# Kernel optimization log

Hardware: AMD Instinct MI355X
Metric: run time of the kernel (lower is better)

The kernel has to match this reference:

```python
import jax, jax.numpy as jnp
import numpy as np

N = 100000   # nodes
E = 800000   # edges
F_IN = 16
H = 64       # hidden_dim
L = 4        # num_layers
CD = 8       # contrastive_dim
BN_EPS = 1e-5


def setup_inputs() -> dict:
    key = jax.random.key(0)
    ks = jax.random.split(key, 20)
    s = 0.05
    return {
        "x": jax.random.normal(ks[0], (N, F_IN), jnp.float32),
        "edge_index": jax.random.randint(ks[1], (2, E), 0, N, jnp.int64),
        "batch": jnp.zeros((N,), jnp.int64),
        "enc_w1": jax.random.normal(ks[2], (F_IN, H), jnp.float32) * s,
        "enc_b1": jnp.zeros((H,), jnp.float32),
        "enc_w2": jax.random.normal(ks[3], (H, H), jnp.float32) * s,
        "enc_b2": jnp.zeros((H,), jnp.float32),
        "conv_w": jax.random.normal(ks[4], (L, 2 * H, H), jnp.float32) * s,
        "conv_b": jnp.zeros((L, H), jnp.float32),
        "bn_gamma": jnp.ones((L, H), jnp.float32),
        "bn_beta": jnp.zeros((L, H), jnp.float32),
        "out_w1": jax.random.normal(ks[5], (H, 64), jnp.float32) * s,
        "out_b1": jnp.zeros((64,), jnp.float32),
        "out_w2": jax.random.normal(ks[6], (64, 32), jnp.float32) * s,
        "out_b2": jnp.zeros((32,), jnp.float32),
        "out_w3": jax.random.normal(ks[7], (32, CD), jnp.float32) * s,
        "out_b3": jnp.zeros((CD,), jnp.float32),
    }


def _forward(x, edge_index, enc_w1, enc_b1, enc_w2, enc_b2,
             conv_w, conv_b, bn_gamma, bn_beta,
             out_w1, out_b1, out_w2, out_b2, out_w3, out_b3):
    row, col = edge_index[0], edge_index[1]
    # lc_encode: Linear+ELU, Linear+ELU
    h = jax.nn.elu(x @ enc_w1 + enc_b1)
    feats = jax.nn.elu(h @ enc_w2 + enc_b2)  # (N, H)

    ones = jnp.ones((E, 1), feats.dtype)
    counts = jnp.clip(jax.ops.segment_sum(ones, row, num_segments=N), 1.0)  # (N,1)
    bn_scale = 1.0 / jnp.sqrt(1.0 + BN_EPS)  # eval-mode BN: running_mean=0, running_var=1

    for i in range(L):
        xc = feats[row]               # gather centers (E, H)
        xn = feats[col]               # gather neighbors (E, H)
        ef = jnp.concatenate([xc, xn - xc], axis=-1)      # (E, 2H)
        e = jax.nn.elu(ef @ conv_w[i] + conv_b[i])        # Linear + ELU
        e = (e * bn_scale) * bn_gamma[i] + bn_beta[i]     # BatchNorm (eval); Dropout is identity
        agg = jax.ops.segment_sum(e, row, num_segments=N) / counts
        feats = agg + feats  # residual in Net.forward

    # output head (Dropout identity in eval)
    o = jax.nn.elu(feats @ out_w1 + out_b1)
    o = jax.nn.elu(o @ out_w2 + out_b2)
    return o @ out_w3 + out_b3  # (N, CD)


def reference(x, edge_index, batch, enc_w1, enc_b1, enc_w2, enc_b2,
              conv_w, conv_b, bn_gamma, bn_beta,
              out_w1, out_b1, out_w2, out_b2, out_w3, out_b3):
    out = _forward(x, edge_index, enc_w1, enc_b1, enc_w2, enc_b2,
                   conv_w, conv_b, bn_gamma, bn_beta,
                   out_w1, out_b1, out_w2, out_b2, out_w3, out_b3)
    return (out, batch)
```

## Files before the change

### kernel.cpp

```cpp
#include <hip/hip_runtime.h>

#define NN 100000
#define NE 800000
#define FIN 16
#define H 64
#define NL 4
#define CDIM 8
#define NT 1563
#define NAB 782
#define ROWS_PER_OWN 12500
#define ECHUNK 2048
#define NCHUNK ((NE + ECHUNK - 1) / ECHUNK)
#define CAP 32
#define HOT 8
#define SPILL (CAP - HOT)

typedef __attribute__((ext_vector_type(8))) short bf16x8;
typedef __attribute__((ext_vector_type(4))) float f32x4;

__device__ __forceinline__ float elu(float x) { return x > 0.f ? x : __expf(x) - 1.f; }
__device__ __forceinline__ float4 elu4(float4 v) {
    return make_float4(elu(v.x), elu(v.y), elu(v.z), elu(v.w));
}

__device__ __forceinline__ unsigned short f2bf(float x) {
    union { float f; unsigned int u; } v; v.f = x;
    unsigned int r = v.u + 0x7fffu + ((v.u >> 16) & 1u);
    return (unsigned short)(r >> 16);
}
__device__ __forceinline__ float u2f(unsigned int u) {
    union { unsigned int u; float f; } v; v.u = u;
    return v.f;
}

__global__ __launch_bounds__(256) void k_scatter(const int* __restrict__ row,
                                                 const int* __restrict__ col,
                                                 int* cnt, int* __restrict__ hot,
                                                 int* __restrict__ spill,
                                                 const float* __restrict__ convw,
                                                 unsigned short* __restrict__ WT) {
    if (blockIdx.x >= NCHUNK * 8) {
        int t = (blockIdx.x - NCHUNK * 8) * 256 + threadIdx.x;
        int i = t >> 11;
        int rem = t & 2047;
        int j = rem >> 4;
        int kg = rem & 15;
        const float* W = convw + (size_t)i * 2 * H * H;
        float v[4];
#pragma unroll
        for (int q = 0; q < 4; q++) {
            int k = kg * 4 + q;
            if (j < 64) v[q] = W[k * 64 + j] - W[(64 + k) * 64 + j];
            else        v[q] = W[(64 + k) * 64 + (j - 64)];
        }
        ushort4 p;
        p.x = f2bf(v[0]); p.y = f2bf(v[1]); p.z = f2bf(v[2]); p.w = f2bf(v[3]);
        *(ushort4*)&WT[(size_t)i * 8192 + j * 64 + kg * 4] = p;
        return;
    }
    int owner = blockIdx.x & 7;
    int chunk = blockIdx.x >> 3;
    int lo = owner * ROWS_PER_OWN, hi = lo + ROWS_PER_OWN;
    int base = chunk * ECHUNK;
    int end = base + ECHUNK; if (end > NE) end = NE;
    for (int e = base + threadIdx.x; e < end; e += 256) {
        int r = row[e];
        if (r >= lo && r < hi) {
            int p = atomicAdd(&cnt[r], 1);
            if (p < HOT) hot[(size_t)r * HOT + p] = col[e];
            else if (p < CAP) spill[(size_t)r * SPILL + (p - HOT)] = col[e];
        }
    }
}

__global__ __launch_bounds__(256) void k_enc(const float* __restrict__ x,
                                             const float* __restrict__ w1,
                                             const float* __restrict__ b1,
                                             const float* __restrict__ w2,
                                             const float* __restrict__ b2,
                                             float* __restrict__ feats,
                                             int* __restrict__ cnt) {
    __shared__ __align__(16) float xs[64 * 16];
    __shared__ __align__(16) float w1s[16 * 64];
    __shared__ __align__(16) float ws[64 * 64];
    __shared__ __align__(16) float fs[64 * 68];
    int tid = threadIdx.x;
    int base = blockIdx.x * 64;
    {
        int gid = blockIdx.x * 256 + tid;
        if (gid < NN) cnt[gid] = 0;
    }
    {
        size_t ei = (size_t)base * FIN + tid * 4;
        size_t emax = (size_t)NN * FIN - 4;
        if (ei > emax) ei = emax;
        *(float4*)&xs[tid * 4] = *(const float4*)&x[ei];
    }
    ((float4*)w1s)[tid] = ((const float4*)w1)[tid];
#pragma unroll
    for (int r = 0; r < 4; r++) ((float4*)ws)[tid + 256 * r] = ((const float4*)w2)[tid + 256 * r];
    __syncthreads();

    int wave = tid >> 6, j = tid & 63;
    float bb1 = b1[j];
    for (int i = 0; i < 16; i++) {
        int nl = i * 4 + wave;
        float acc = bb1;
#pragma unroll
        for (int k = 0; k < FIN; k++) acc += xs[nl * FIN + k] * w1s[k * 64 + j];
        fs[nl * 68 + j] = elu(acc);
    }
    __syncthreads();

    int cg = tid & 15, ng = tid >> 4;
    int c0 = cg * 4;
    float4 bb = ((const float4*)b2)[cg];
    float4 acc[4];
    acc[0] = bb; acc[1] = bb; acc[2] = bb; acc[3] = bb;
#pragma unroll 2
    for (int kq = 0; kq < 16; kq++) {
        int k0 = kq * 4;
        float4 w0 = *(const float4*)&ws[(k0 + 0) * 64 + c0];
        float4 w1v = *(const float4*)&ws[(k0 + 1) * 64 + c0];
        float4 w2v = *(const float4*)&ws[(k0 + 2) * 64 + c0];
        float4 w3v = *(const float4*)&ws[(k0 + 3) * 64 + c0];
#pragma unroll
        for (int m = 0; m < 4; m++) {
            float4 f = *(const float4*)&fs[(ng * 4 + m) * 68 + k0];
            acc[m].x += f.x * w0.x + f.y * w1v.x + f.z * w2v.x + f.w * w3v.x;
            acc[m].y += f.x * w0.y + f.y * w1v.y + f.z * w2v.y + f.w * w3v.y;
            acc[m].z += f.x * w0.z + f.y * w1v.z + f.z * w2v.z + f.w * w3v.z;
            acc[m].w += f.x * w0.w + f.y * w1v.w + f.z * w2v.w + f.w * w3v.w;
        }
    }
#pragma unroll
    for (int m = 0; m < 4; m++) {
        int n = base + ng * 4 + m;
        if (n < NN) *(float4*)&feats[(size_t)n * 64 + c0] = elu4(acc[m]);
    }
}

__global__ __launch_bounds__(256) void k_ab(const float* __restrict__ feats,
                                            const unsigned short* __restrict__ WT,
                                            const float* __restrict__ convb,
                                            unsigned short* __restrict__ Am,
                                            unsigned short* __restrict__ Bm) {
    int tid = threadIdx.x;
    int wave = tid >> 6, l = tid & 63;
    int lr = l & 15;
    int lk = l >> 4;
    int nb = blockIdx.x * 128 + wave * 32;

    bf16x8 wf[8][2];
#pragma unroll
    for (int ct = 0; ct < 8; ct++)
#pragma unroll
        for (int kt = 0; kt < 2; kt++)
            wf[ct][kt] = *(const bf16x8*)&WT[(ct * 16 + lr) * 64 + kt * 32 + lk * 8];

    f32x4 acc[2][8];
#pragma unroll
    for (int ct = 0; ct < 4; ct++) {
        float4 bq = *(const float4*)&convb[ct * 16 + lk * 4];
        f32x4 bv; bv[0] = bq.x; bv[1] = bq.y; bv[2] = bq.z; bv[3] = bq.w;
        f32x4 z = (f32x4)(0.0f);
        acc[0][ct] = bv; acc[1][ct] = bv;
        acc[0][ct + 4] = z; acc[1][ct + 4] = z;
    }

#pragma unroll
    for (int nt = 0; nt < 2; nt++) {
        int n = nb + nt * 16 + lr; if (n >= NN) n = NN - 1;
        bf16x8 ff[2];
#pragma unroll
        for (int kt = 0; kt < 2; kt++) {
            float4 f0 = *(const float4*)&feats[(size_t)n * 64 + kt * 32 + lk * 8];
            float4 f1 = *(const float4*)&feats[(size_t)n * 64 + kt * 32 + lk * 8 + 4];
            bf16x8 t;
            t[0] = (short)f2bf(f0.x); t[1] = (short)f2bf(f0.y);
            t[2] = (short)f2bf(f0.z); t[3] = (short)f2bf(f0.w);
            t[4] = (short)f2bf(f1.x); t[5] = (short)f2bf(f1.y);
            t[6] = (short)f2bf(f1.z); t[7] = (short)f2bf(f1.w);
            ff[kt] = t;
        }
#pragma unroll
        for (int ct = 0; ct < 8; ct++) {
            acc[nt][ct] = __builtin_amdgcn_mfma_f32_16x16x32_bf16(wf[ct][0], ff[0], acc[nt][ct], 0, 0, 0);
            acc[nt][ct] = __builtin_amdgcn_mfma_f32_16x16x32_bf16(wf[ct][1], ff[1], acc[nt][ct], 0, 0, 0);
        }
    }

#pragma unroll
    for (int nt = 0; nt < 2; nt++) {
        int n = nb + nt * 16 + lr;
        if (n < NN) {
#pragma unroll
            for (int ct = 0; ct < 8; ct++) {
                ushort4 p;
                p.x = f2bf(acc[nt][ct][0]); p.y = f2bf(acc[nt][ct][1]);
                p.z = f2bf(acc[nt][ct][2]); p.w = f2bf(acc[nt][ct][3]);
                unsigned short* dst = (ct < 4) ? Am : Bm;
                int wc = (ct & 3) * 16 + lk * 4;
                *(ushort4*)&dst[(size_t)n * 64 + wc] = p;
            }
        }
    }
}

__global__ __launch_bounds__(256) void k_gather(const unsigned short* __restrict__ Am,
                                                const unsigned short* __restrict__ Bm,
                                                const int* __restrict__ cnt,
                                                const int* __restrict__ hot,
                                                const int* __restrict__ spill,
                                                const float* __restrict__ gamma,
                                                const float* __restrict__ beta,
                                                float* __restrict__ feats) {
    int tid = threadIdx.x;
    int wave = tid >> 6, lane = tid & 63;
    int half = lane >> 5, l = lane & 31;
    int n = blockIdx.x * 8 + wave * 2 + half;
    int g = l >> 3;
    int cq = l & 7, c0 = cq * 8;
    int deg = cnt[n];
    if (deg > CAP) deg = CAP;
    int mycol = (l < HOT) ? hot[(size_t)n * HOT + l]
                          : spill[(size_t)n * SPILL + (l - HOT)];
    uint4 rawA = *(const uint4*)&Am[(size_t)n * H + c0];
    float4 a0 = make_float4(u2f(rawA.x << 16), u2f(rawA.x & 0xffff0000u),
                            u2f(rawA.y << 16), u2f(rawA.y & 0xffff0000u));
    float4 a1 = make_float4(u2f(rawA.z << 16), u2f(rawA.z & 0xffff0000u),
                            u2f(rawA.w << 16), u2f(rawA.w & 0xffff0000u));
    float4 f0, f1;
    if (g == 0) {
        f0 = *(const float4*)&feats[(size_t)n * H + c0];
        f1 = *(const float4*)&feats[(size_t)n * H + c0 + 4];
    }
    float4 acc0 = make_float4(0.f, 0.f, 0.f, 0.f);
    float4 acc1 = make_float4(0.f, 0.f, 0.f, 0.f);
    for (int p0 = 0; p0 < deg; p0 += 4) {
        int p = p0 + g;
        bool valid = p < deg;
        int pc = valid ? p : (deg - 1);
        int c = __shfl(mycol, (half << 5) + pc);
        uint4 raw = *(const uint4*)&Bm[(size_t)c * H + c0];
        float4 b0 = make_float4(u2f(raw.x << 16), u2f(raw.x & 0xffff0000u),
                                u2f(raw.y << 16), u2f(raw.y & 0xffff0000u));
        float4 b1 = make_float4(u2f(raw.z << 16), u2f(raw.z & 0xffff0000u),
                                u2f(raw.w << 16), u2f(raw.w & 0xffff0000u));
        float4 v0 = elu4(make_float4(a0.x + b0.x, a0.y + b0.y, a0.z + b0.z, a0.w + b0.w));
        float4 v1 = elu4(make_float4(a1.x + b1.x, a1.y + b1.y, a1.z + b1.z, a1.w + b1.w));
        if (valid) {
            acc0.x += v0.x; acc0.y += v0.y; acc0.z += v0.z; acc0.w += v0.w;
            acc1.x += v1.x; acc1.y += v1.y; acc1.z += v1.z; acc1.w += v1.w;
        }
    }
#pragma unroll
    for (int d = 8; d < 32; d <<= 1) {
        acc0.x += __shfl_xor(acc0.x, d); acc0.y += __shfl_xor(acc0.y, d);
        acc0.z += __shfl_xor(acc0.z, d); acc0.w += __shfl_xor(acc0.w, d);
        acc1.x += __shfl_xor(acc1.x, d); acc1.y += __shfl_xor(acc1.y, d);
        acc1.z += __shfl_xor(acc1.z, d); acc1.w += __shfl_xor(acc1.w, d);
    }
    if (g == 0 && deg > 0) {
        const float bs = 0.99999500003749968750f;
        float inv = bs / (float)deg;
        float4 gm0 = *(const float4*)&gamma[c0];
        float4 gm1 = *(const float4*)&gamma[c0 + 4];
        float4 bt0 = *(const float4*)&beta[c0];
        float4 bt1 = *(const float4*)&beta[c0 + 4];
        f0.x += acc0.x * gm0.x * inv + bt0.x;
        f0.y += acc0.y * gm0.y * inv + bt0.y;
        f0.z += acc0.z * gm0.z * inv + bt0.z;
        f0.w += acc0.w * gm0.w * inv + bt0.w;
        f1.x += acc1.x * gm1.x * inv + bt1.x;
        f1.y += acc1.y * gm1.y * inv + bt1.y;
        f1.z += acc1.z * gm1.z * inv + bt1.z;
        f1.w += acc1.w * gm1.w * inv + bt1.w;
        *(float4*)&feats[(size_t)n * H + c0] = f0;
        *(float4*)&feats[(size_t)n * H + c0 + 4] = f1;
    }
}

__global__ __launch_bounds__(256) void k_head(const float* __restrict__ feats,
                                              const float* __restrict__ w1,
                                              const float* __restrict__ b1,
                                              const float* __restrict__ w2,
                                              const float* __restrict__ b2,
                                              const float* __restrict__ w3,
                                              const float* __restrict__ b3,
                                              const int* __restrict__ batch,
                                              float* __restrict__ out,
                                              float* __restrict__ out2) {
    __shared__ __align__(16) float fs[64 * 68];
    __shared__ __align__(16) float w1s[64 * 64];
    __shared__ __align__(16) float o1s[64 * 68];
    __shared__ __align__(16) float w2s[64 * 32];
    __shared__ __align__(16) float w3s[32 * 8];
    int tid = threadIdx.x;
    int base = blockIdx.x * 64;
#pragma unroll
    for (int r = 0; r < 4; r++) {
        int idx = tid + 256 * r;
        ((float4*)w1s)[idx] = ((const float4*)w1)[idx];
        int rw = idx >> 4, cc = idx & 15;
        int n = base + rw; if (n >= NN) n = NN - 1;
        *(float4*)&fs[rw * 68 + cc * 4] = *(const float4*)&feats[(size_t)n * 64 + cc * 4];
    }
    ((float4*)w2s)[tid] = ((const float4*)w2)[tid];
    ((float4*)w2s)[tid + 256] = ((const float4*)w2)[tid + 256];
    if (tid < 64) ((float4*)w3s)[tid] = ((const float4*)w3)[tid];
    if (tid < 64) {
        int n = base + tid;
        if (n < NN) out2[n] = (float)batch[n];
    }
    __syncthreads();

    int cg = tid & 15, ng = tid >> 4;
    int c0 = cg * 4;
    {
        float4 bb = ((const float4*)b1)[cg];
        float4 acc[4];
        acc[0] = bb; acc[1] = bb; acc[2] = bb; acc[3] = bb;
#pragma unroll 2
        for (int kq = 0; kq < 16; kq++) {
            int k0 = kq * 4;
            float4 w0 = *(const float4*)&w1s[(k0 + 0) * 64 + c0];
            float4 w1v = *(const float4*)&w1s[(k0 + 1) * 64 + c0];
            float4 w2v = *(const float4*)&w1s[(k0 + 2) * 64 + c0];
            float4 w3v = *(const float4*)&w1s[(k0 + 3) * 64 + c0];
#pragma unroll
            for (int m = 0; m < 4; m++) {
                float4 f = *(const float4*)&fs[(ng * 4 + m) * 68 + k0];
                acc[m].x += f.x * w0.x + f.y * w1v.x + f.z * w2v.x + f.w * w3v.x;
                acc[m].y += f.x * w0.y + f.y * w1v.y + f.z * w2v.y + f.w * w3v.y;
                acc[m].z += f.x * w0.z + f.y * w1v.z + f.z * w2v.z + f.w * w3v.z;
                acc[m].w += f.x * w0.w + f.y * w1v.w + f.z * w2v.w + f.w * w3v.w;
            }
        }
        __syncthreads();
#pragma unroll
        for (int m = 0; m < 4; m++)
            *(float4*)&o1s[(ng * 4 + m) * 68 + c0] = elu4(acc[m]);
    }
    __syncthreads();

    float* o2s = fs;
    {
        int cg2 = tid & 7, ng2 = tid >> 3;
        int c20 = cg2 * 4;
        float4 bb = ((const float4*)b2)[cg2];
        float4 acc[2];
        acc[0] = bb; acc[1] = bb;
#pragma unroll 2
        for (int kq = 0; kq < 16; kq++) {
            int k0 = kq * 4;
            float4 w0 = *(const float4*)&w2s[(k0 + 0) * 32 + c20];
            float4 w1v = *(const float4*)&w2s[(k0 + 1) * 32 + c20];
            float4 w2v = *(const float4*)&w2s[(k0 + 2) * 32 + c20];
            float4 w3v = *(const float4*)&w2s[(k0 + 3) * 32 + c20];
#pragma unroll
            for (int m = 0; m < 2; m++) {
                float4 f = *(const float4*)&o1s[(ng2 * 2 + m) * 68 + k0];
                acc[m].x += f.x * w0.x + f.y * w1v.x + f.z * w2v.x + f.w * w3v.x;
                acc[m].y += f.x * w0.y + f.y * w1v.y + f.z * w2v.y + f.w * w3v.y;
                acc[m].z += f.x * w0.z + f.y * w1v.z + f.z * w2v.z + f.w * w3v.z;
                acc[m].w += f.x * w0.w + f.y * w1v.w + f.z * w2v.w + f.w * w3v.w;
            }
        }
#pragma unroll
        for (int m = 0; m < 2; m++)
            *(float4*)&o2s[(ng2 * 2 + m) * 40 + c20] = elu4(acc[m]);
    }
    __syncthreads();

    if (tid < 128) {
        int n3 = tid >> 1, c30 = (tid & 1) * 4;
        float4 acc = ((const float4*)b3)[tid & 1];
#pragma unroll 2
        for (int kq = 0; kq < 8; kq++) {
            int k0 = kq * 4;
            float4 w0 = *(const float4*)&w3s[(k0 + 0) * 8 + c30];
            float4 w1v = *(const float4*)&w3s[(k0 + 1) * 8 + c30];
            float4 w2v = *(const float4*)&w3s[(k0 + 2) * 8 + c30];
            float4 w3v = *(const float4*)&w3s[(k0 + 3) * 8 + c30];
            float4 f = *(const float4*)&o2s[n3 * 40 + k0];
            acc.x += f.x * w0.x + f.y * w1v.x + f.z * w2v.x + f.w * w3v.x;
            acc.y += f.x * w0.y + f.y * w1v.y + f.z * w2v.y + f.w * w3v.y;
            acc.z += f.x * w0.z + f.y * w1v.z + f.z * w2v.z + f.w * w3v.z;
            acc.w += f.x * w0.w + f.y * w1v.w + f.z * w2v.w + f.w * w3v.w;
        }
        int n = base + n3;
        if (n < NN) *(float4*)&out[(size_t)n * 8 + c30] = acc;
    }
}

extern "C" void kernel_launch(void* const* d_in, const int* in_sizes, int n_in,
                              void* d_out, int out_size, void* d_ws, size_t ws_size,
                              hipStream_t stream) {
    const float* x = (const float*)d_in[0];
    const int* edge_index = (const int*)d_in[1];
    const int* batch = (const int*)d_in[2];
    const float* enc_w1 = (const float*)d_in[3];
    const float* enc_b1 = (const float*)d_in[4];
    const float* enc_w2 = (const float*)d_in[5];
    const float* enc_b2 = (const float*)d_in[6];
    const float* conv_w = (const float*)d_in[7];
    const float* conv_b = (const float*)d_in[8];
    const float* bn_gamma = (const float*)d_in[9];
    const float* bn_beta = (const float*)d_in[10];
    const float* out_w1 = (const float*)d_in[11];
    const float* out_b1 = (const float*)d_in[12];
    const float* out_w2 = (const float*)d_in[13];
    const float* out_b2 = (const float*)d_in[14];
    const float* out_w3 = (const float*)d_in[15];
    const float* out_b3 = (const float*)d_in[16];

    const int* row = edge_index;
    const int* col = edge_index + NE;

    float* feats = (float*)d_ws;
    unsigned short* Abuf = (unsigned short*)(feats + (size_t)NN * H);
    unsigned short* Bbuf = Abuf + (size_t)NN * H;
    int* cnt = (int*)(Bbuf + (size_t)NN * H);
    int* hot = cnt + NN;
    int* spill = hot + (size_t)NN * HOT;
    unsigned short* WT = (unsigned short*)(spill + (size_t)NN * SPILL);

    float* out = (float*)d_out;

    k_enc<<<NT, 256, 0, stream>>>(x, enc_w1, enc_b1, enc_w2, enc_b2, feats, cnt);
    k_scatter<<<NCHUNK * 8 + 32, 256, 0, stream>>>(row, col, cnt, hot, spill, conv_w, WT);

    for (int i = 0; i < NL; i++) {
        k_ab<<<NAB, 256, 0, stream>>>(feats, WT + (size_t)i * 8192,
                                      conv_b + (size_t)i * H, Abuf, Bbuf);
        k_gather<<<NN / 8, 256, 0, stream>>>(Abuf, Bbuf, cnt, hot, spill,
                                             bn_gamma + (size_t)i * H,
                                             bn_beta + (size_t)i * H, feats);
    }

    k_head<<<NT, 256, 0, stream>>>(feats, out_w1, out_b1, out_w2, out_b2,
                                   out_w3, out_b3, batch, out,
                                   out + (size_t)NN * CDIM);
}
```

Measured before the change: 383.6 us.

## Fuse neighbor aggregation with next layer's A/B projection, double-buffering B

A new kernel, k_gab, does layer i's neighbor gather, mean, BN and residual update for a 128-node tile. After a barrier it computes layer i+1's A/B bf16 projections for the same tile. B is ping-ponged between two buffers because other blocks still read the old B as neighbor values, while A and feats are only touched by their owning tile. The conv weight transpose also moves from k_scatter into extra blocks of k_enc. This saves a few launches and one re-read of feats per layer. The cost is far fewer, longer-running blocks in the gather phase, each wave walking 32 nodes serially, which may hide less gather latency.

```diff
diff --git a/kernel.cpp b/kernel.cpp
--- a/kernel.cpp
+++ b/kernel.cpp
@@ -11,6 +11,7 @@
 #define ROWS_PER_OWN 12500
 #define ECHUNK 2048
 #define NCHUNK ((NE + ECHUNK - 1) / ECHUNK)
+#define NSC (NCHUNK * 8)
 #define CAP 32
 #define HOT 8
 #define SPILL (CAP - HOT)
@@ -36,28 +37,7 @@
 __global__ __launch_bounds__(256) void k_scatter(const int* __restrict__ row,
                                                  const int* __restrict__ col,
                                                  int* cnt, int* __restrict__ hot,
-                                                 int* __restrict__ spill,
-                                                 const float* __restrict__ convw,
-                                                 unsigned short* __restrict__ WT) {
-    if (blockIdx.x >= NCHUNK * 8) {
-        int t = (blockIdx.x - NCHUNK * 8) * 256 + threadIdx.x;
-        int i = t >> 11;
-        int rem = t & 2047;
-        int j = rem >> 4;
-        int kg = rem & 15;
-        const float* W = convw + (size_t)i * 2 * H * H;
-        float v[4];
-#pragma unroll
-        for (int q = 0; q < 4; q++) {
-            int k = kg * 4 + q;
-            if (j < 64) v[q] = W[k * 64 + j] - W[(64 + k) * 64 + j];
-            else        v[q] = W[(64 + k) * 64 + (j - 64)];
-        }
-        ushort4 p;
-        p.x = f2bf(v[0]); p.y = f2bf(v[1]); p.z = f2bf(v[2]); p.w = f2bf(v[3]);
-        *(ushort4*)&WT[(size_t)i * 8192 + j * 64 + kg * 4] = p;
-        return;
-    }
+                                                 int* __restrict__ spill) {
     int owner = blockIdx.x & 7;
     int chunk = blockIdx.x >> 3;
     int lo = owner * ROWS_PER_OWN, hi = lo + ROWS_PER_OWN;
@@ -79,12 +59,33 @@
                                              const float* __restrict__ w2,
                                              const float* __restrict__ b2,
                                              float* __restrict__ feats,
-                                             int* __restrict__ cnt) {
+                                             int* __restrict__ cnt,
+                                             const float* __restrict__ convw,
+                                             unsigned short* __restrict__ WT) {
+    int tid = threadIdx.x;
+    if (blockIdx.x >= NT) {
+        int t = (blockIdx.x - NT) * 256 + tid;
+        int i = t >> 11;
+        int rem = t & 2047;
+        int j = rem >> 4;
+        int kg = rem & 15;
+        const float* W = convw + (size_t)i * 2 * H * H;
+        float v[4];
+#pragma unroll
+        for (int q = 0; q < 4; q++) {
+            int k = kg * 4 + q;
+            if (j < 64) v[q] = W[k * 64 + j] - W[(64 + k) * 64 + j];
+            else        v[q] = W[(64 + k) * 64 + (j - 64)];
+        }
+        ushort4 p;
+        p.x = f2bf(v[0]); p.y = f2bf(v[1]); p.z = f2bf(v[2]); p.w = f2bf(v[3]);
+        *(ushort4*)&WT[(size_t)i * 8192 + j * 64 + kg * 4] = p;
+        return;
+    }
     __shared__ __align__(16) float xs[64 * 16];
     __shared__ __align__(16) float w1s[16 * 64];
     __shared__ __align__(16) float ws[64 * 64];
     __shared__ __align__(16) float fs[64 * 68];
-    int tid = threadIdx.x;
     int base = blockIdx.x * 64;
     {
         int gid = blockIdx.x * 256 + tid;
@@ -140,17 +141,12 @@
     }
 }
 
-__global__ __launch_bounds__(256) void k_ab(const float* __restrict__ feats,
-                                            const unsigned short* __restrict__ WT,
-                                            const float* __restrict__ convb,
-                                            unsigned short* __restrict__ Am,
-                                            unsigned short* __restrict__ Bm) {
-    int tid = threadIdx.x;
-    int wave = tid >> 6, l = tid & 63;
-    int lr = l & 15;
-    int lk = l >> 4;
-    int nb = blockIdx.x * 128 + wave * 32;
-
+__device__ __forceinline__ void ab_body(int nb, int lr, int lk,
+                                        const float* __restrict__ feats,
+                                        const unsigned short* __restrict__ WT,
+                                        const float* __restrict__ convb,
+                                        unsigned short* __restrict__ Am,
+                                        unsigned short* __restrict__ Bm) {
     bf16x8 wf[8][2];
 #pragma unroll
     for (int ct = 0; ct < 8; ct++)
@@ -205,6 +201,103 @@
             }
         }
     }
+}
+
+__global__ __launch_bounds__(256) void k_ab(const float* __restrict__ feats,
+                                            const unsigned short* __restrict__ WT,
+                                            const float* __restrict__ convb,
+                                            unsigned short* __restrict__ Am,
+                                            unsigned short* __restrict__ Bm) {
+    int tid = threadIdx.x;
+    int wave = tid >> 6, l = tid & 63;
+    ab_body(blockIdx.x * 128 + wave * 32, l & 15, l >> 4, feats, WT, convb, Am, Bm);
+}
+
+__global__ __launch_bounds__(256) void k_gab(const unsigned short* __restrict__ Brd,
+                                             unsigned short* __restrict__ Am,
+                                             unsigned short* __restrict__ Bwr,
+                                             const int* __restrict__ cnt,
+                                             const int* __restrict__ hot,
+                                             const int* __restrict__ spill,
+                                             const float* __restrict__ gamma,
+                                             const float* __restrict__ beta,
+                                             float* __restrict__ feats,
+                                             const unsigned short* __restrict__ WT,
+                                             const float* __restrict__ convb) {
+    int tid = threadIdx.x;
+    int wave = tid >> 6, lane = tid & 63;
+    int half = lane >> 5, l = lane & 31;
+    int g = l >> 3;
+    int cq = l & 7, c0 = cq * 8;
+    int nb = blockIdx.x * 128 + wave * 32;
+
+    const float bs = 0.99999500003749968750f;
+    float4 gm0 = *(const float4*)&gamma[c0];
+    float4 gm1 = *(const float4*)&gamma[c0 + 4];
+    float4 bt0 = *(const float4*)&beta[c0];
+    float4 bt1 = *(const float4*)&beta[c0 + 4];
+
+    for (int j = 0; j < 16; j++) {
+        int n = nb + j * 2 + half;
+        if (n >= NN) continue;
+        int deg = cnt[n];
+        if (deg > CAP) deg = CAP;
+        int mycol = (l < HOT) ? hot[(size_t)n * HOT + l]
+                              : spill[(size_t)n * SPILL + (l - HOT)];
+        uint4 rawA = *(const uint4*)&Am[(size_t)n * H + c0];
+        float4 a0 = make_float4(u2f(rawA.x << 16), u2f(rawA.x & 0xffff0000u),
+                                u2f(rawA.y << 16), u2f(rawA.y & 0xffff0000u));
+        float4 a1 = make_float4(u2f(rawA.z << 16), u2f(rawA.z & 0xffff0000u),
+                                u2f(rawA.w << 16), u2f(rawA.w & 0xffff0000u));
+        float4 f0, f1;
+        if (g == 0) {
+            f0 = *(const float4*)&feats[(size_t)n * H + c0];
+            f1 = *(const float4*)&feats[(size_t)n * H + c0 + 4];
+        }
+        float4 acc0 = make_float4(0.f, 0.f, 0.f, 0.f);
+        float4 acc1 = make_float4(0.f, 0.f, 0.f, 0.f);
+        for (int p0 = 0; p0 < deg; p0 += 4) {
+            int p = p0 + g;
+            bool valid = p < deg;
+            int pc = valid ? p : (deg - 1);
+            int c = __shfl(mycol, (half << 5) + pc);
+            uint4 raw = *(const uint4*)&Brd[(size_t)c * H + c0];
+            float4 b0 = make_float4(u2f(raw.x << 16), u2f(raw.x & 0xffff0000u),
+                                    u2f(raw.y << 16), u2f(raw.y & 0xffff0000u));
+            float4 b1 = make_float4(u2f(raw.z << 16), u2f(raw.z & 0xffff0000u),
+                                    u2f(raw.w << 16), u2f(raw.w & 0xffff0000u));
+            float4 v0 = elu4(make_float4(a0.x + b0.x, a0.y + b0.y, a0.z + b0.z, a0.w + b0.w));
+            float4 v1 = elu4(make_float4(a1.x + b1.x, a1.y + b1.y, a1.z + b1.z, a1.w + b1.w));
+            if (valid) {
+                acc0.x += v0.x; acc0.y += v0.y; acc0.z += v0.z; acc0.w += v0.w;
+                acc1.x += v1.x; acc1.y += v1.y; acc1.z += v1.z; acc1.w += v1.w;
+            }
+        }
+#pragma unroll
+        for (int d = 8; d < 32; d <<= 1) {
+            acc0.x += __shfl_xor(acc0.x, d); acc0.y += __shfl_xor(acc0.y, d);
+            acc0.z += __shfl_xor(acc0.z, d); acc0.w += __shfl_xor(acc0.w, d);
+            acc1.x += __shfl_xor(acc1.x, d); acc1.y += __shfl_xor(acc1.y, d);
+            acc1.z += __shfl_xor(acc1.z, d); acc1.w += __shfl_xor(acc1.w, d);
+        }
+        if (g == 0 && deg > 0) {
+            float inv = bs / (float)deg;
+            f0.x += acc0.x * gm0.x * inv + bt0.x;
+            f0.y += acc0.y * gm0.y * inv + bt0.y;
+            f0.z += acc0.z * gm0.z * inv + bt0.z;
+            f0.w += acc0.w * gm0.w * inv + bt0.w;
+            f1.x += acc1.x * gm1.x * inv + bt1.x;
+            f1.y += acc1.y * gm1.y * inv + bt1.y;
+            f1.z += acc1.z * gm1.z * inv + bt1.z;
+            f1.w += acc1.w * gm1.w * inv + bt1.w;
+            *(float4*)&feats[(size_t)n * H + c0] = f0;
+            *(float4*)&feats[(size_t)n * H + c0 + 4] = f1;
+        }
+    }
+
+    __syncthreads();
+
+    ab_body(nb, lane & 15, lane >> 4, feats, WT, convb, Am, Bwr);
 }
 
 __global__ __launch_bounds__(256) void k_gather(const unsigned short* __restrict__ Am,
@@ -420,24 +513,33 @@
 
     float* feats = (float*)d_ws;
     unsigned short* Abuf = (unsigned short*)(feats + (size_t)NN * H);
-    unsigned short* Bbuf = Abuf + (size_t)NN * H;
-    int* cnt = (int*)(Bbuf + (size_t)NN * H);
+    unsigned short* Bbuf0 = Abuf + (size_t)NN * H;
+    unsigned short* Bbuf1 = Bbuf0 + (size_t)NN * H;
+    int* cnt = (int*)(Bbuf1 + (size_t)NN * H);
     int* hot = cnt + NN;
     int* spill = hot + (size_t)NN * HOT;
     unsigned short* WT = (unsigned short*)(spill + (size_t)NN * SPILL);
 
     float* out = (float*)d_out;
 
-    k_enc<<<NT, 256, 0, stream>>>(x, enc_w1, enc_b1, enc_w2, enc_b2, feats, cnt);
-    k_scatter<<<NCHUNK * 8 + 32, 256, 0, stream>>>(row, col, cnt, hot, spill, conv_w, WT);
-
-    for (int i = 0; i < NL; i++) {
-        k_ab<<<NAB, 256, 0, stream>>>(feats, WT + (size_t)i * 8192,
-                                      conv_b + (size_t)i * H, Abuf, Bbuf);
-        k_gather<<<NN / 8, 256, 0, stream>>>(Abuf, Bbuf, cnt, hot, spill,
-                                             bn_gamma + (size_t)i * H,
-                                             bn_beta + (size_t)i * H, feats);
-    }
+    k_enc<<<NT + 32, 256, 0, stream>>>(x, enc_w1, enc_b1, enc_w2, enc_b2, feats, cnt,
+                                       conv_w, WT);
+    k_scatter<<<NSC, 256, 0, stream>>>(row, col, cnt, hot, spill);
+
+    k_ab<<<NAB, 256, 0, stream>>>(feats, WT, conv_b, Abuf, Bbuf0);
+
+    unsigned short* Brd = Bbuf0;
+    unsigned short* Bwr = Bbuf1;
+    for (int i = 0; i < NL - 1; i++) {
+        k_gab<<<NAB, 256, 0, stream>>>(Brd, Abuf, Bwr, cnt, hot, spill,
+                                       bn_gamma + (size_t)i * H, bn_beta + (size_t)i * H,
+                                       feats, WT + (size_t)(i + 1) * 8192,
+                                       conv_b + (size_t)(i + 1) * H);
+        unsigned short* t = Brd; Brd = Bwr; Bwr = t;
+    }
+    k_gather<<<NN / 8, 256, 0, stream>>>(Abuf, Brd, cnt, hot, spill,
+                                         bn_gamma + (size_t)(NL - 1) * H,
+                                         bn_beta + (size_t)(NL - 1) * H, feats);
 
     k_head<<<NT, 256, 0, stream>>>(feats, out_w1, out_b1, out_w2, out_b2,
                                    out_w3, out_b3, batch, out,
```

Measured after the change: 496.4 us. +29.4%, slower.
